# Kernel optimization log

Measured on AMD Instinct MI355X. Metric: run time of the kernel, lower is better.

## Reference

```python
import jax, jax.numpy as jnp
import numpy as np
import math

B, S, D, H, WD = 8, 2048, 512, 8, 64
DK = D // H


def setup_inputs() -> dict:
    k = jax.random.key(0)
    ks = jax.random.split(k, 16)
    s = 0.02
    return {
        "query": jax.random.normal(ks[0], (B, S, D), jnp.float32),
        "key": jax.random.normal(ks[1], (B, S, D), jnp.float32),
        "value": jax.random.normal(ks[2], (B, S, D), jnp.float32),
        "mask": jax.random.randint(ks[3], (B, S), 0, 2, jnp.int32),
        "segment_weights": jax.random.uniform(ks[4], (B, S, S), jnp.float32),
        # torch Linear weights: [out_features, in_features]
        "Wq": jax.random.normal(ks[5], (D, D), jnp.float32) * s,
        "bq": jnp.zeros((D,), jnp.float32),
        "Wk": jax.random.normal(ks[6], (D, D), jnp.float32) * s,
        "bk": jnp.zeros((D,), jnp.float32),
        "Wv": jax.random.normal(ks[7], (D, D), jnp.float32) * s,
        "bv": jnp.zeros((D,), jnp.float32),
        "Wo": jax.random.normal(ks[8], (D, D), jnp.float32) * s,
        "bo": jnp.zeros((D,), jnp.float32),
        "Wl": jax.random.normal(ks[9], (WD, 1), jnp.float32) * 0.1,
        "bl": jnp.zeros((WD,), jnp.float32),
        "Wr": jax.random.normal(ks[10], (1, WD), jnp.float32) * 0.1,
        "br": jnp.zeros((1,), jnp.float32),
    }


def reference(query, key, value, mask, segment_weights,
              Wq, bq, Wk, bk, Wv, bv, Wo, bo, Wl, bl, Wr, br):
    nb = query.shape[0]
    # segment bias MLP: 1 -> WD -> 1 with leaky_relu(0.2)
    sw = 1.0 / jnp.log(jnp.float32(math.e) + segment_weights)  # [B,S,S]
    hmid = jax.nn.leaky_relu(sw[..., None] * Wl[:, 0] + bl, negative_slope=0.2)  # [B,S,S,WD]
    bias = (hmid @ Wr.T + br)[..., 0]  # [B,S,S]

    def proj(x, W, b):
        return (x @ W.T + b).reshape(nb, -1, H, DK).transpose(0, 2, 1, 3)  # [B,H,S,DK]

    q = proj(query, Wq, bq)
    k = proj(key, Wk, bk)
    v = proj(value, Wv, bv)

    scores = jnp.einsum("bhqd,bhkd->bhqk", q, k) / jnp.float32(math.sqrt(DK))
    scores = scores + bias[:, None]  # broadcast over heads
    # mask [B,S] -> [B,1,S,1]: masks query rows (as in original)
    scores = jnp.where(mask[:, None, :, None] == 0, jnp.float32(-1e9), scores)
    p = jax.nn.softmax(scores, axis=-1)
    x = jnp.einsum("bhqk,bhkd->bhqd", p, v)
    x = x.transpose(0, 2, 1, 3).reshape(nb, -1, H * DK)
    return x @ Wo.T + bo
```

## Files before the change

kernel.cpp:

```cpp
#include <hip/hip_runtime.h>
#include <stdint.h>

#define Bb 8
#define Ss 2048
#define Dd 512
#define Hh 8

typedef unsigned short u16;
typedef __attribute__((ext_vector_type(8))) short s16x8;
typedef __attribute__((ext_vector_type(4))) unsigned short u16x4;
typedef __attribute__((ext_vector_type(4))) float f32x4;
typedef __attribute__((ext_vector_type(2))) float f32x2;

__device__ __forceinline__ u16 f2bf(float f){
  unsigned u = __float_as_uint(f);
  return (u16)((u + 0x7fffu + ((u>>16)&1u)) >> 16);
}

__device__ __forceinline__ unsigned cvtpk_bf16(float lo, float hi){
  unsigned r;
  asm("v_cvt_pk_bf16_f32 %0, %1, %2" : "=v"(r) : "v"(lo), "v"(hi));
  return r;
}

__device__ __forceinline__ void gl_lds16(const void* g, void* l){
  __builtin_amdgcn_global_load_lds((const __attribute__((address_space(1))) unsigned int*)g,
                                   (__attribute__((address_space(3))) unsigned int*)l, 16, 0, 0);
}

#define MFMA32(a,b,c) __builtin_amdgcn_mfma_f32_16x16x32_bf16(a,b,c,0,0,0)

__global__ __launch_bounds__(256) void castw(const float* __restrict__ a, const float* __restrict__ b,
                                             const float* __restrict__ c, const float* __restrict__ d,
                                             u16* __restrict__ o){
  int i = blockIdx.x*256 + threadIdx.x;
  const float* src = (i < 65536) ? a : (i < 131072) ? b : (i < 196608) ? c : d;
  int off = (i & 65535) << 2;
  f32x4 v = *(const f32x4*)(src + off);
  u16x4 r;
  #pragma unroll
  for(int j = 0; j < 4; j++) r[j] = f2bf(v[j]);
  *(u16x4*)(o + ((size_t)(i >> 16) << 18) + off) = r;
}

__global__ void prep(const float* __restrict__ Wl, const float* __restrict__ bl,
                     const float* __restrict__ Wr, const float* __restrict__ br,
                     float* __restrict__ consts){
  int w = threadIdx.x;
  float wl = Wl[w], blv = bl[w], wr = Wr[w];
  float h0 = 0.75f*wl + blv; h0 = h0 > 0.f ? h0 : 0.2f*h0;
  float h1 = 1.00f*wl + blv; h1 = h1 > 0.f ? h1 : 0.2f*h1;
  float f0 = wr*h0, f1 = wr*h1;
  #pragma unroll
  for(int off = 32; off > 0; off >>= 1){
    f0 += __shfl_down(f0, off);
    f1 += __shfl_down(f1, off);
  }
  if(w == 0){
    const float L2E = 1.4426950408889634f;
    float brv = br[0];
    float F0 = f0 + brv, F1 = f1 + brv;
    float C1 = (F1 - F0) * 4.0f;
    float C0 = F0 - 0.75f*C1;
    consts[0] = C1 * L2E * L2E;
    consts[1] = C0 * L2E;
  }
}

template<int MODE>
__global__ __launch_bounds__(256) void gemm_t(const void* __restrict__ Ap, const u16* __restrict__ W,
                                              const float* __restrict__ bias, void* __restrict__ Cp){
  __shared__ __align__(16) u16 As[128*32];
  __shared__ __align__(16) u16 Bs[128*32];
  const int t = threadIdx.x;
  const int lane = t & 63, wv = t >> 6;
  const int quad = lane >> 4, l15 = lane & 15;
  const int m0 = blockIdx.x * 128, n0 = blockIdx.y * 128;
  const int R = (wv >> 1) * 64, Cc = (wv & 1) * 64;
  f32x4 acc[4][4] = {};
  for(int kb = 0; kb < 512; kb += 32){
    __syncthreads();
    #pragma unroll
    for(int i = 0; i < 2; i++){
      int u  = i*256 + t;
      int m  = u >> 2;
      int cc = (u & 3) ^ ((m >> 1) & 3);
      if (MODE == 2){
        gl_lds16((const u16*)Ap + (size_t)(m0 + m)*512 + kb + cc*8, As + (size_t)(i*256 + wv*64)*8);
      } else {
        const float* src = (const float*)Ap + (size_t)(m0 + m)*512 + kb + cc*8;
        f32x4 v0 = *(const f32x4*)src;
        f32x4 v1 = *(const f32x4*)(src + 4);
        s16x8 cv;
        #pragma unroll
        for(int r2 = 0; r2 < 4; r2++){ cv[r2] = (short)f2bf(v0[r2]); cv[4+r2] = (short)f2bf(v1[r2]); }
        *(s16x8*)(As + (size_t)u*8) = cv;
      }
      gl_lds16(W + (size_t)(n0 + m)*512 + kb + cc*8, Bs + (size_t)(i*256 + wv*64)*8);
    }
    __syncthreads();
    s16x8 af[4], bfr[4];
    #pragma unroll
    for(int mi = 0; mi < 4; mi++){
      int m = R + mi*16 + l15;
      int u = (m << 2) | (quad ^ ((m >> 1) & 3));
      af[mi] = *(const s16x8*)(As + (size_t)u*8);
    }
    #pragma unroll
    for(int ni = 0; ni < 4; ni++){
      int n = Cc + ni*16 + l15;
      int u = (n << 2) | (quad ^ ((n >> 1) & 3));
      bfr[ni] = *(const s16x8*)(Bs + (size_t)u*8);
    }
    #pragma unroll
    for(int mi = 0; mi < 4; mi++)
      #pragma unroll
      for(int ni = 0; ni < 4; ni++)
        acc[mi][ni] = MFMA32(af[mi], bfr[ni], acc[mi][ni]);
  }
  #pragma unroll
  for(int ni = 0; ni < 4; ni++){
    int col = n0 + Cc + ni*16 + l15;
    float bv = bias[col];
    int hh = col >> 6;
    int mi2 = (col >> 4) & 3, al15v = col & 15;
    int w6 = col & 63, ks = w6 >> 5, aqk = (w6 >> 3) & 3, jk = w6 & 7;
    #pragma unroll
    for(int mi = 0; mi < 4; mi++){
      int row0 = m0 + R + mi*16 + quad*4;
      if (MODE == 1){
        int bb2 = row0 >> 11, tok = row0 & 2047, kb2 = tok >> 5, kl = tok & 31;
        int aq = kl >> 3, jb = kl & 7;
        u16x4 o;
        #pragma unroll
        for(int r = 0; r < 4; r++) o[r] = f2bf(acc[mi][ni][r] + bv);
        size_t off = (((((size_t)bb2*64 + kb2)*8 + hh)*4 + mi2)*64 + (size_t)(aq*16 + al15v))*8 + jb;
        *(u16x4*)((u16*)Cp + off) = o;
      } else {
        #pragma unroll
        for(int r = 0; r < 4; r++){
          float v = acc[mi][ni][r] + bv;
          int row = row0 + r;
          if (MODE == 2)      ((float*)Cp)[(size_t)row*512 + col] = v;
          else if (MODE == 3){
            int bb2 = row >> 11, tok = row & 2047, kb2 = tok >> 5, kl = tok & 31;
            int kmi = (kl >> 2) & 1;
            int al15 = 4*(kl >> 3) + (kl & 3);
            size_t off = (((((size_t)bb2*64 + kb2)*8 + hh)*4 + (ks*2 + kmi))*64 + (size_t)(aqk*16 + al15))*8 + jk;
            ((u16*)Cp)[off] = f2bf(v);
          }
          else                ((u16*)Cp)[(size_t)row*512 + col] = f2bf(v);
        }
      }
    }
  }
}

__global__ __launch_bounds__(512, 4) void attn(const u16* __restrict__ qp, const u16* __restrict__ kf_g,
                                               const u16* __restrict__ vf_g, const float* __restrict__ seg,
                                               const int* __restrict__ mask, const float* __restrict__ consts,
                                               u16* __restrict__ xo){
  __shared__ __align__(16) float bias_s[2][32*36];
  const int t = threadIdx.x;
  const int lane = t & 63, h = t >> 6;
  const int quad = lane >> 4, l15 = lane & 15;
  const int id = (blockIdx.x & 7) * 64 + (blockIdx.x >> 3);
  const int b = id >> 6, q0 = (id & 63) * 32;
  const float C1 = consts[0], C0 = consts[1];

  s16x8 qf[2][2];
  #pragma unroll
  for(int ni = 0; ni < 2; ni++){
    const u16* qrow = qp + (size_t)(b*Ss + q0 + ni*16 + l15)*Dd + h*64;
    qf[ni][0] = *(const s16x8*)(qrow + quad*8);
    qf[ni][1] = *(const s16x8*)(qrow + 32 + quad*8);
  }
  float mk[2];
  #pragma unroll
  for(int ni = 0; ni < 2; ni++)
    mk[ni] = (mask[b*Ss + q0 + ni*16 + l15] == 0) ? 0.0f : 1.0f;

  f32x4 ot[4][2] = {};
  float lsum[2] = {0.f, 0.f};

  const int sq = t >> 4, sk = (t & 15) * 2;
  const float* segptr = seg + ((size_t)b*Ss + (size_t)(q0 + sq))*Ss + sk;

  const u16* kfp = kf_g + (size_t)b*1048576 + h*2048 + (size_t)lane*8;
  const u16* vfp = vf_g + (size_t)b*1048576 + h*2048 + (size_t)lane*8;

  f32x2 raw = *(const f32x2*)(segptr);
  f32x2 bvreg;
  #pragma unroll
  for(int j = 0; j < 2; j++)
    bvreg[j] = C1 * __builtin_amdgcn_rcpf(__log2f(2.718281828459045f + raw[j])) + C0;

  for(int k0 = 0; k0 < Ss; k0 += 32){
    float* bs = bias_s[(k0 >> 5) & 1];

    const u16* kfb = kfp + (size_t)k0*512;
    s16x8 kf[2][2];
    kf[0][0] = *(const s16x8*)(kfb);
    kf[1][0] = *(const s16x8*)(kfb + 512);
    kf[0][1] = *(const s16x8*)(kfb + 1024);
    kf[1][1] = *(const s16x8*)(kfb + 1536);
    *(f32x2*)(bs + sq*36 + sk) = bvreg;
    if (k0 + 32 < Ss) raw = *(const f32x2*)(segptr + k0 + 32);

    asm volatile("s_waitcnt lgkmcnt(0)" ::: "memory");
    __builtin_amdgcn_s_barrier();
    __builtin_amdgcn_sched_barrier(0);

    f32x4 st[2][2] = {};
    #pragma unroll
    for(int ks = 0; ks < 2; ks++)
      #pragma unroll
      for(int mi = 0; mi < 2; mi++)
        #pragma unroll
        for(int ni = 0; ni < 2; ni++)
          st[mi][ni] = MFMA32(kf[mi][ks], qf[ni][ks], st[mi][ni]);

    const u16* vfb = vfp + (size_t)k0*512;
    s16x8 vf[4];
    #pragma unroll
    for(int mi2 = 0; mi2 < 4; mi2++)
      vf[mi2] = *(const s16x8*)(vfb + mi2*512);

    union { unsigned u[4]; s16x8 v; } P[2];
    #pragma unroll
    for(int mi = 0; mi < 2; mi++)
      #pragma unroll
      for(int ni = 0; ni < 2; ni++){
        f32x4 bb = *(const f32x4*)(bs + (ni*16 + l15)*36 + quad*8 + mi*4);
        f32x4 s = st[mi][ni] * 0.18033688011112042f + bb;
        s *= mk[ni];
        float p[4];
        #pragma unroll
        for(int r = 0; r < 4; r++){
          float sv = __builtin_amdgcn_fmed3f(s[r], -30.f, 30.f);
          p[r] = __builtin_amdgcn_exp2f(sv);
          lsum[ni] += p[r];
        }
        P[ni].u[mi*2 + 0] = cvtpk_bf16(p[0], p[1]);
        P[ni].u[mi*2 + 1] = cvtpk_bf16(p[2], p[3]);
      }

    #pragma unroll
    for(int mi2 = 0; mi2 < 4; mi2++)
      #pragma unroll
      for(int ni = 0; ni < 2; ni++)
        ot[mi2][ni] = MFMA32(vf[mi2], P[ni].v, ot[mi2][ni]);

    if (k0 + 32 < Ss){
      #pragma unroll
      for(int j = 0; j < 2; j++)
        bvreg[j] = C1 * __builtin_amdgcn_rcpf(__log2f(2.718281828459045f + raw[j])) + C0;
    }
  }

  float rl[2];
  #pragma unroll
  for(int ni = 0; ni < 2; ni++){
    float l = lsum[ni];
    l += __shfl_xor(l, 16);
    l += __shfl_xor(l, 32);
    rl[ni] = 1.0f / l;
  }

  #pragma unroll
  for(int ni = 0; ni < 2; ni++)
    #pragma unroll
    for(int mi2 = 0; mi2 < 4; mi2++){
      u16x4 o;
      #pragma unroll
      for(int r = 0; r < 4; r++) o[r] = f2bf(ot[mi2][ni][r] * rl[ni]);
      *(u16x4*)(xo + (size_t)(b*Ss + q0 + ni*16 + l15)*Dd + h*64 + mi2*16 + quad*4) = o;
    }
}

extern "C" void kernel_launch(void* const* d_in, const int* in_sizes, int n_in,
                              void* d_out, int out_size, void* d_ws, size_t ws_size,
                              hipStream_t stream){
  const float* query = (const float*)d_in[0];
  const float* key   = (const float*)d_in[1];
  const float* value = (const float*)d_in[2];
  const int*   mask  = (const int*)d_in[3];
  const float* seg   = (const float*)d_in[4];
  const float* Wq = (const float*)d_in[5];  const float* bq = (const float*)d_in[6];
  const float* Wk = (const float*)d_in[7];  const float* bk = (const float*)d_in[8];
  const float* Wv = (const float*)d_in[9];  const float* bv = (const float*)d_in[10];
  const float* Wo = (const float*)d_in[11]; const float* bo = (const float*)d_in[12];
  const float* Wl = (const float*)d_in[13]; const float* bl = (const float*)d_in[14];
  const float* Wr = (const float*)d_in[15]; const float* br = (const float*)d_in[16];

  char* ws = (char*)d_ws;
  float* consts = (float*)ws;
  u16* Wc  = (u16*)(ws + 4096);
  u16* qp  = (u16*)(ws + ((size_t)4  << 20));
  u16* kfb = (u16*)(ws + ((size_t)20 << 20));
  u16* vfb = (u16*)(ws + ((size_t)36 << 20));
  u16* xo  = qp;
  const size_t WN = (size_t)512*512;

  castw<<<1024, 256, 0, stream>>>(Wq, Wk, Wv, Wo, Wc);
  prep<<<1, 64, 0, stream>>>(Wl, bl, Wr, br, consts);
  gemm_t<0><<<dim3(128,4), 256, 0, stream>>>(query, Wc + 0*WN, bq, qp);
  gemm_t<3><<<dim3(128,4), 256, 0, stream>>>(key,   Wc + 1*WN, bk, kfb);
  gemm_t<1><<<dim3(128,4), 256, 0, stream>>>(value, Wc + 2*WN, bv, vfb);
  attn<<<512, 512, 0, stream>>>(qp, kfb, vfb, seg, mask, consts, xo);
  gemm_t<2><<<dim3(128,4), 256, 0, stream>>>(xo, Wc + 3*WN, bo, d_out);
}
```

Measured before the change: 478.7 us.

## Halve attention query tile to 16 rows and double block count for occupancy

Each attention block now covers 16 query rows instead of 32, so the grid doubles to 1024 blocks and launch bounds target 8 waves per SIMD. Per-thread register state (Q fragments, score and output accumulators) is halved. The mask is folded into the scale and the bias, and the softmax clamp is removed. In exchange, K and V tiles are reloaded twice as often per query row, which doubles K/V global traffic, and dropping the clamp leaves the exponent unbounded.

```diff
diff --git a/kernel.cpp b/kernel.cpp
--- a/kernel.cpp
+++ b/kernel.cpp
@@ -156,69 +156,56 @@
   }
 }
 
-__global__ __launch_bounds__(512, 4) void attn(const u16* __restrict__ qp, const u16* __restrict__ kf_g,
+__global__ __launch_bounds__(512, 8) void attn(const u16* __restrict__ qp, const u16* __restrict__ kf_g,
                                                const u16* __restrict__ vf_g, const float* __restrict__ seg,
                                                const int* __restrict__ mask, const float* __restrict__ consts,
                                                u16* __restrict__ xo){
-  __shared__ __align__(16) float bias_s[2][32*36];
+  __shared__ __align__(16) float bias_s[2][16*36];
   const int t = threadIdx.x;
   const int lane = t & 63, h = t >> 6;
   const int quad = lane >> 4, l15 = lane & 15;
-  const int id = (blockIdx.x & 7) * 64 + (blockIdx.x >> 3);
-  const int b = id >> 6, q0 = (id & 63) * 32;
+  const int id = (blockIdx.x & 7) * 128 + (blockIdx.x >> 3);
+  const int b = id >> 7, q0 = (id & 127) * 16;
   const float C1 = consts[0], C0 = consts[1];
 
-  s16x8 qf[2][2];
-  #pragma unroll
-  for(int ni = 0; ni < 2; ni++){
-    const u16* qrow = qp + (size_t)(b*Ss + q0 + ni*16 + l15)*Dd + h*64;
-    qf[ni][0] = *(const s16x8*)(qrow + quad*8);
-    qf[ni][1] = *(const s16x8*)(qrow + 32 + quad*8);
-  }
-  float mk[2];
-  #pragma unroll
-  for(int ni = 0; ni < 2; ni++)
-    mk[ni] = (mask[b*Ss + q0 + ni*16 + l15] == 0) ? 0.0f : 1.0f;
-
-  f32x4 ot[4][2] = {};
-  float lsum[2] = {0.f, 0.f};
-
-  const int sq = t >> 4, sk = (t & 15) * 2;
+  const u16* qrow = qp + (size_t)(b*Ss + q0 + l15)*Dd + h*64;
+  s16x8 qf0 = *(const s16x8*)(qrow + quad*8);
+  s16x8 qf1 = *(const s16x8*)(qrow + 32 + quad*8);
+  const float cmk = (mask[b*Ss + q0 + l15] == 0) ? 0.0f : 0.18033688011112042f;
+
+  f32x4 ot[4] = {};
+  float lsum = 0.f;
+
+  const int sq = t >> 5, sk = t & 31;
+  const float mrow = (mask[b*Ss + q0 + sq] == 0) ? 0.0f : 1.0f;
   const float* segptr = seg + ((size_t)b*Ss + (size_t)(q0 + sq))*Ss + sk;
 
   const u16* kfp = kf_g + (size_t)b*1048576 + h*2048 + (size_t)lane*8;
   const u16* vfp = vf_g + (size_t)b*1048576 + h*2048 + (size_t)lane*8;
 
-  f32x2 raw = *(const f32x2*)(segptr);
-  f32x2 bvreg;
-  #pragma unroll
-  for(int j = 0; j < 2; j++)
-    bvreg[j] = C1 * __builtin_amdgcn_rcpf(__log2f(2.718281828459045f + raw[j])) + C0;
+  float raw = *segptr;
+  float bvreg = (C1 * __builtin_amdgcn_rcpf(__log2f(2.718281828459045f + raw)) + C0) * mrow;
 
   for(int k0 = 0; k0 < Ss; k0 += 32){
     float* bs = bias_s[(k0 >> 5) & 1];
 
     const u16* kfb = kfp + (size_t)k0*512;
-    s16x8 kf[2][2];
-    kf[0][0] = *(const s16x8*)(kfb);
-    kf[1][0] = *(const s16x8*)(kfb + 512);
-    kf[0][1] = *(const s16x8*)(kfb + 1024);
-    kf[1][1] = *(const s16x8*)(kfb + 1536);
-    *(f32x2*)(bs + sq*36 + sk) = bvreg;
-    if (k0 + 32 < Ss) raw = *(const f32x2*)(segptr + k0 + 32);
+    s16x8 kf00 = *(const s16x8*)(kfb);
+    s16x8 kf10 = *(const s16x8*)(kfb + 512);
+    s16x8 kf01 = *(const s16x8*)(kfb + 1024);
+    s16x8 kf11 = *(const s16x8*)(kfb + 1536);
+    bs[sq*36 + sk] = bvreg;
+    if (k0 + 32 < Ss) raw = segptr[k0 + 32];
 
     asm volatile("s_waitcnt lgkmcnt(0)" ::: "memory");
     __builtin_amdgcn_s_barrier();
     __builtin_amdgcn_sched_barrier(0);
 
-    f32x4 st[2][2] = {};
-    #pragma unroll
-    for(int ks = 0; ks < 2; ks++)
-      #pragma unroll
-      for(int mi = 0; mi < 2; mi++)
-        #pragma unroll
-        for(int ni = 0; ni < 2; ni++)
-          st[mi][ni] = MFMA32(kf[mi][ks], qf[ni][ks], st[mi][ni]);
+    f32x4 st0 = {}, st1 = {};
+    st0 = MFMA32(kf00, qf0, st0);
+    st1 = MFMA32(kf10, qf0, st1);
+    st0 = MFMA32(kf01, qf1, st0);
+    st1 = MFMA32(kf11, qf1, st1);
 
     const u16* vfb = vfp + (size_t)k0*512;
     s16x8 vf[4];
@@ -226,56 +213,44 @@
     for(int mi2 = 0; mi2 < 4; mi2++)
       vf[mi2] = *(const s16x8*)(vfb + mi2*512);
 
-    union { unsigned u[4]; s16x8 v; } P[2];
-    #pragma unroll
-    for(int mi = 0; mi < 2; mi++)
+    union { unsigned u[4]; s16x8 v; } P;
+    {
+      f32x4 bb0 = *(const f32x4*)(bs + l15*36 + quad*8);
+      f32x4 bb1 = *(const f32x4*)(bs + l15*36 + quad*8 + 4);
+      float p[8];
       #pragma unroll
-      for(int ni = 0; ni < 2; ni++){
-        f32x4 bb = *(const f32x4*)(bs + (ni*16 + l15)*36 + quad*8 + mi*4);
-        f32x4 s = st[mi][ni] * 0.18033688011112042f + bb;
-        s *= mk[ni];
-        float p[4];
-        #pragma unroll
-        for(int r = 0; r < 4; r++){
-          float sv = __builtin_amdgcn_fmed3f(s[r], -30.f, 30.f);
-          p[r] = __builtin_amdgcn_exp2f(sv);
-          lsum[ni] += p[r];
-        }
-        P[ni].u[mi*2 + 0] = cvtpk_bf16(p[0], p[1]);
-        P[ni].u[mi*2 + 1] = cvtpk_bf16(p[2], p[3]);
+      for(int r = 0; r < 4; r++){
+        p[r]   = __builtin_amdgcn_exp2f(st0[r] * cmk + bb0[r]);
+        p[4+r] = __builtin_amdgcn_exp2f(st1[r] * cmk + bb1[r]);
       }
+      #pragma unroll
+      for(int r = 0; r < 8; r++) lsum += p[r];
+      P.u[0] = cvtpk_bf16(p[0], p[1]);
+      P.u[1] = cvtpk_bf16(p[2], p[3]);
+      P.u[2] = cvtpk_bf16(p[4], p[5]);
+      P.u[3] = cvtpk_bf16(p[6], p[7]);
+    }
 
     #pragma unroll
     for(int mi2 = 0; mi2 < 4; mi2++)
-      #pragma unroll
-      for(int ni = 0; ni < 2; ni++)
-        ot[mi2][ni] = MFMA32(vf[mi2], P[ni].v, ot[mi2][ni]);
-
-    if (k0 + 32 < Ss){
-      #pragma unroll
-      for(int j = 0; j < 2; j++)
-        bvreg[j] = C1 * __builtin_amdgcn_rcpf(__log2f(2.718281828459045f + raw[j])) + C0;
-    }
-  }
-
-  float rl[2];
-  #pragma unroll
-  for(int ni = 0; ni < 2; ni++){
-    float l = lsum[ni];
-    l += __shfl_xor(l, 16);
-    l += __shfl_xor(l, 32);
-    rl[ni] = 1.0f / l;
-  }
-
-  #pragma unroll
-  for(int ni = 0; ni < 2; ni++)
-    #pragma unroll
-    for(int mi2 = 0; mi2 < 4; mi2++){
-      u16x4 o;
-      #pragma unroll
-      for(int r = 0; r < 4; r++) o[r] = f2bf(ot[mi2][ni][r] * rl[ni]);
-      *(u16x4*)(xo + (size_t)(b*Ss + q0 + ni*16 + l15)*Dd + h*64 + mi2*16 + quad*4) = o;
-    }
+      ot[mi2] = MFMA32(vf[mi2], P.v, ot[mi2]);
+
+    if (k0 + 32 < Ss)
+      bvreg = (C1 * __builtin_amdgcn_rcpf(__log2f(2.718281828459045f + raw)) + C0) * mrow;
+  }
+
+  float l = lsum;
+  l += __shfl_xor(l, 16);
+  l += __shfl_xor(l, 32);
+  const float rl = 1.0f / l;
+
+  #pragma unroll
+  for(int mi2 = 0; mi2 < 4; mi2++){
+    u16x4 o;
+    #pragma unroll
+    for(int r = 0; r < 4; r++) o[r] = f2bf(ot[mi2][r] * rl);
+    *(u16x4*)(xo + (size_t)(b*Ss + q0 + l15)*Dd + h*64 + mi2*16 + quad*4) = o;
+  }
 }
 
 extern "C" void kernel_launch(void* const* d_in, const int* in_sizes, int n_in,
@@ -307,6 +282,6 @@
   gemm_t<0><<<dim3(128,4), 256, 0, stream>>>(query, Wc + 0*WN, bq, qp);
   gemm_t<3><<<dim3(128,4), 256, 0, stream>>>(key,   Wc + 1*WN, bk, kfb);
   gemm_t<1><<<dim3(128,4), 256, 0, stream>>>(value, Wc + 2*WN, bv, vfb);
-  attn<<<512, 512, 0, stream>>>(qp, kfb, vfb, seg, mask, consts, xo);
+  attn<<<1024, 512, 0, stream>>>(qp, kfb, vfb, seg, mask, consts, xo);
   gemm_t<2><<<dim3(128,4), 256, 0, stream>>>(xo, Wc + 3*WN, bo, d_out);
 }
```

New measurement: 567.5 us. +18.6%, slower.
